# Optimization experiments

Measured on AMD Instinct MI355X. Metric: run time of the kernel, lower is better.

Reference implementation:

```python
import jax, jax.numpy as jnp
import numpy as np

IN_FEATURES = 4096
B, S = 4, 4096


def setup_inputs() -> dict:
    key = jax.random.key(0)
    k1, k2, k3 = jax.random.split(key, 3)
    input_1 = jax.random.normal(k1, (B, S, IN_FEATURES), dtype=jnp.float32)
    input_2 = jax.random.normal(k2, (B, S, IN_FEATURES), dtype=jnp.float32)
    weight = jax.random.uniform(k3, (IN_FEATURES,), dtype=jnp.float32)
    return {"input_1": input_1, "input_2": input_2, "weight": weight}


def reference(input_1, input_2, weight):
    # Original: linear(input_1, diag(w)) + linear(input_2, diag(1-w)).
    # diag(w) is symmetric, so x @ diag(w).T == x * w (elementwise broadcast
    # over the last feature axis) -- identical math without the O(n^2) matmul.
    return input_1 * weight + input_2 * (1.0 - weight)
```

## Files before the change

### kernel.cpp

```cpp
#include <hip/hip_runtime.h>


__global__ __launch_bounds__(256) void merger_kernel(
    const float4* __restrict__ a,
    const float4* __restrict__ b,
    const float4* __restrict__ w,
    float4* __restrict__ out,
    int n4) {
    const int f4mask = 1023;
    int idx = blockIdx.x * blockDim.x + threadIdx.x;
    int stride = gridDim.x * blockDim.x;
    for (int i = idx; i < n4; i += stride) {
        float4 av = a[i];
        float4 bv = b[i];
        float4 wv = w[i & f4mask];
        float4 o;
        o.x = av.x * wv.x + bv.x * (1.0f - wv.x);
        o.y = av.y * wv.y + bv.y * (1.0f - wv.y);
        o.z = av.z * wv.z + bv.z * (1.0f - wv.z);
        o.w = av.w * wv.w + bv.w * (1.0f - wv.w);
        out[i] = o;
    }
}

extern "C" void kernel_launch(void* const* d_in, const int* in_sizes, int n_in,
                              void* d_out, int out_size, void* d_ws, size_t ws_size,
                              hipStream_t stream) {
    const float4* a = (const float4*)d_in[0];
    const float4* b = (const float4*)d_in[1];
    const float4* w = (const float4*)d_in[2];
    float4* out = (float4*)d_out;
    int n4 = out_size / 4;

    const int block = 256;
    const int grid = 2048;
    merger_kernel<<<grid, block, 0, stream>>>(a, b, w, out, n4);
}
```

Baseline: 159.4 us.

## Unroll per-row loads with one block per row and nontemporal output stores

Replaces the grid-stride loop with one block per 1024-float4 feature row, where each thread issues four independent loads from each input before computing. This raises the number of memory requests in flight. Outputs are written with nontemporal stores to avoid polluting caches with streaming data. The bounds check is removed, so the kernel assumes the total size is a multiple of the row length.

```diff
diff --git a/kernel.cpp b/kernel.cpp
--- a/kernel.cpp
+++ b/kernel.cpp
@@ -1,38 +1,48 @@
 #include <hip/hip_runtime.h>
 
 
+typedef float fvec4 __attribute__((ext_vector_type(4)));
+
 __global__ __launch_bounds__(256) void merger_kernel(
-    const float4* __restrict__ a,
-    const float4* __restrict__ b,
-    const float4* __restrict__ w,
-    float4* __restrict__ out,
-    int n4) {
-    const int f4mask = 1023;
-    int idx = blockIdx.x * blockDim.x + threadIdx.x;
-    int stride = gridDim.x * blockDim.x;
-    for (int i = idx; i < n4; i += stride) {
-        float4 av = a[i];
-        float4 bv = b[i];
-        float4 wv = w[i & f4mask];
-        float4 o;
-        o.x = av.x * wv.x + bv.x * (1.0f - wv.x);
-        o.y = av.y * wv.y + bv.y * (1.0f - wv.y);
-        o.z = av.z * wv.z + bv.z * (1.0f - wv.z);
-        o.w = av.w * wv.w + bv.w * (1.0f - wv.w);
-        out[i] = o;
-    }
+    const fvec4* __restrict__ a,
+    const fvec4* __restrict__ b,
+    const fvec4* __restrict__ w,
+    fvec4* __restrict__ out) {
+    const int t = threadIdx.x;
+    const int base = blockIdx.x * 1024 + t;
+
+    const fvec4 wv0 = w[t];
+    const fvec4 wv1 = w[t + 256];
+    const fvec4 wv2 = w[t + 512];
+    const fvec4 wv3 = w[t + 768];
+
+    const fvec4 av0 = a[base];
+    const fvec4 av1 = a[base + 256];
+    const fvec4 av2 = a[base + 512];
+    const fvec4 av3 = a[base + 768];
+    const fvec4 bv0 = b[base];
+    const fvec4 bv1 = b[base + 256];
+    const fvec4 bv2 = b[base + 512];
+    const fvec4 bv3 = b[base + 768];
+
+    const fvec4 o0 = av0 * wv0 + bv0 * (1.0f - wv0);
+    const fvec4 o1 = av1 * wv1 + bv1 * (1.0f - wv1);
+    const fvec4 o2 = av2 * wv2 + bv2 * (1.0f - wv2);
+    const fvec4 o3 = av3 * wv3 + bv3 * (1.0f - wv3);
+
+    __builtin_nontemporal_store(o0, &out[base]);
+    __builtin_nontemporal_store(o1, &out[base + 256]);
+    __builtin_nontemporal_store(o2, &out[base + 512]);
+    __builtin_nontemporal_store(o3, &out[base + 768]);
 }
 
 extern "C" void kernel_launch(void* const* d_in, const int* in_sizes, int n_in,
                               void* d_out, int out_size, void* d_ws, size_t ws_size,
                               hipStream_t stream) {
-    const float4* a = (const float4*)d_in[0];
-    const float4* b = (const float4*)d_in[1];
-    const float4* w = (const float4*)d_in[2];
-    float4* out = (float4*)d_out;
-    int n4 = out_size / 4;
-
-    const int block = 256;
-    const int grid = 2048;
-    merger_kernel<<<grid, block, 0, stream>>>(a, b, w, out, n4);
+    const fvec4* a = (const fvec4*)d_in[0];
+    const fvec4* b = (const fvec4*)d_in[1];
+    const fvec4* w = (const fvec4*)d_in[2];
+    fvec4* out = (fvec4*)d_out;
+    const int grid = out_size / (4 * 1024);
+    merger_kernel<<<grid, 256, 0, stream>>>(a, b, w, out);
 }
```

Measured after the change: 139.6 us. -12.4%, faster.
